# Optimization experiments

Measured on AMD Instinct MI355X. Metric: run time of the kernel, lower is better.

The kernel has to match this reference:

```python
import jax, jax.numpy as jnp
import numpy as np

N_NODES = 100000
N_EDGES = 3200000
IN_DIM = 256
OUT_DIM = 256


def setup_inputs() -> dict:
    key = jax.random.key(0)
    k1, k2, k3, k4, k5 = jax.random.split(key, 5)
    x = jax.random.normal(k1, (N_NODES, IN_DIM), dtype=jnp.float32)
    edge_src = jax.random.randint(k2, (N_EDGES,), 0, N_NODES, dtype=jnp.int32)
    edge_dst = jax.random.randint(k3, (N_EDGES,), 0, N_NODES, dtype=jnp.int32)
    # normalized adjacency values (e.g. D^-1/2 A D^-1/2 entries)
    edge_val = jax.random.uniform(k4, (N_EDGES,), dtype=jnp.float32)
    # parameters: uniform(0,1) weight, constant 0.3 bias (matches torch init)
    weight = jax.random.uniform(k5, (IN_DIM, OUT_DIM), dtype=jnp.float32)
    bias = jnp.full((OUT_DIM,), 0.3, dtype=jnp.float32)
    return {"x": x, "edge_src": edge_src, "edge_dst": edge_dst,
            "edge_val": edge_val, "weight": weight, "bias": bias}


def reference(x, edge_src, edge_dst, edge_val, weight, bias):
    # dense feature transform: [N, in] @ [in, out] -> [N, out]
    h = x @ weight
    # sparse adjacency aggregation: out[d] = sum_e val[e] * h[src[e]] for dst[e]==d
    msgs = edge_val[:, None] * h[edge_src]              # [E, out]
    agg = jax.ops.segment_sum(msgs, edge_dst, num_segments=N_NODES)
    return agg + bias
```

## Files before the change

kernel.cpp:

```cpp
#include <hip/hip_runtime.h>

#define FDIM 256
#define BSH 6
#define NBMAX 1600
#define CH 4096
#define NSLOT 7
#define CAPB 2432

typedef __attribute__((ext_vector_type(4))) float f32x4;
typedef __attribute__((ext_vector_type(8))) short bf16x8;
typedef unsigned long long u64;

static __device__ __forceinline__ unsigned short f32_to_bf16_rtn(float f) {
    unsigned u = __builtin_bit_cast(unsigned, f);
    u += 0x7FFFu + ((u >> 16) & 1u);
    return (unsigned short)(u >> 16);
}
static __device__ __forceinline__ float bf16_to_f32(unsigned short s) {
    unsigned u = ((unsigned)s) << 16;
    return __builtin_bit_cast(float, u);
}

__global__ __launch_bounds__(256) void convert_hist_kernel(
    const float* __restrict__ x, unsigned short* __restrict__ xh, long n8,
    const int* __restrict__ dst, int* __restrict__ bucket_counts, int n_edges, int nb,
    const float* __restrict__ W, unsigned short* __restrict__ wfrag) {
    __shared__ int h[NBMAX];
    for (int i = threadIdx.x; i < nb; i += 256) h[i] = 0;
    __syncthreads();

    if (blockIdx.x < 32) {
        int t = blockIdx.x * 256 + threadIdx.x;
        int lane = t & 63;
        int kt   = (t >> 6) & 7;
        int nt   = t >> 9;
        int col  = nt * 16 + (lane & 15);
        int k0   = kt * 32 + 8 * (lane >> 4);
        ushort4 o0, o1;
        o0.x = f32_to_bf16_rtn(W[(k0 + 0) * FDIM + col]);
        o0.y = f32_to_bf16_rtn(W[(k0 + 1) * FDIM + col]);
        o0.z = f32_to_bf16_rtn(W[(k0 + 2) * FDIM + col]);
        o0.w = f32_to_bf16_rtn(W[(k0 + 3) * FDIM + col]);
        o1.x = f32_to_bf16_rtn(W[(k0 + 4) * FDIM + col]);
        o1.y = f32_to_bf16_rtn(W[(k0 + 5) * FDIM + col]);
        o1.z = f32_to_bf16_rtn(W[(k0 + 6) * FDIM + col]);
        o1.w = f32_to_bf16_rtn(W[(k0 + 7) * FDIM + col]);
        ((ushort4*)(wfrag + (size_t)t * 8))[0] = o0;
        ((ushort4*)(wfrag + (size_t)t * 8))[1] = o1;
    }

    long i = (long)blockIdx.x * 256 + threadIdx.x;
    long stride = (long)gridDim.x * 256;
    for (long p = i; p < n8; p += stride) {
        const float4* q = (const float4*)(x + p * 8);
        float4 a = q[0], b = q[1];
        ushort4 o0, o1;
        o0.x = f32_to_bf16_rtn(a.x); o0.y = f32_to_bf16_rtn(a.y);
        o0.z = f32_to_bf16_rtn(a.z); o0.w = f32_to_bf16_rtn(a.w);
        o1.x = f32_to_bf16_rtn(b.x); o1.y = f32_to_bf16_rtn(b.y);
        o1.z = f32_to_bf16_rtn(b.z); o1.w = f32_to_bf16_rtn(b.w);
        ((ushort4*)(xh + p * 8))[0] = o0;
        ((ushort4*)(xh + p * 8))[1] = o1;
    }
    for (long p = i; p < n_edges; p += stride) atomicAdd(&h[dst[p] >> BSH], 1);
    __syncthreads();
    for (int b = threadIdx.x; b < nb; b += 256)
        if (h[b]) atomicAdd(&bucket_counts[b], h[b]);
}

__global__ __launch_bounds__(1024) void scan_buckets_kernel(const int* __restrict__ counts,
                                                            int* __restrict__ base,
                                                            int* __restrict__ cursor, int nb) {
    __shared__ int s[1024];
    int t = threadIdx.x;
    int i0 = 2 * t, i1 = 2 * t + 1;
    int v0 = (i0 < nb) ? counts[i0] : 0;
    int v1 = (i1 < nb) ? counts[i1] : 0;
    s[t] = v0 + v1;
    __syncthreads();
    #pragma unroll
    for (int off = 1; off < 1024; off <<= 1) {
        int u = (t >= off) ? s[t - off] : 0;
        __syncthreads();
        s[t] += u;
        __syncthreads();
    }
    int excl = s[t] - (v0 + v1);
    if (i0 < nb) { base[i0] = excl;      cursor[i0] = excl; }
    if (i1 < nb) { base[i1] = excl + v0; cursor[i1] = excl + v0; }
}

__global__ __launch_bounds__(256) void bin_kernel(
    const int* __restrict__ src, const int* __restrict__ dst, const float* __restrict__ val,
    int* __restrict__ bucket_cursor, u64* __restrict__ binned, int n_edges, int nb) {
    __shared__ int hist[NBMAX];
    __shared__ int gbase[NBMAX];
    __shared__ int sbase[NBMAX];
    __shared__ int scan_s[256];
    __shared__ u64 stage[CH];
    __shared__ unsigned short bos[CH];

    const int t = threadIdx.x;
    const int chunk0 = blockIdx.x * CH;
    const int m = min(CH, n_edges - chunk0);

    for (int b = t; b < nb; b += 256) hist[b] = 0;
    __syncthreads();
    for (int i = t; i < m; i += 256) atomicAdd(&hist[dst[chunk0 + i] >> BSH], 1);
    __syncthreads();
    for (int b = t; b < nb; b += 256) {
        int c = hist[b];
        gbase[b] = c ? atomicAdd(&bucket_cursor[b], c) : 0;
    }
    int loc[NSLOT]; int sum = 0;
    #pragma unroll
    for (int k = 0; k < NSLOT; ++k) {
        int b = t * NSLOT + k;
        int c = (b < nb) ? hist[b] : 0;
        loc[k] = sum; sum += c;
    }
    scan_s[t] = sum;
    __syncthreads();
    #pragma unroll
    for (int off = 1; off < 256; off <<= 1) {
        int u = (t >= off) ? scan_s[t - off] : 0;
        __syncthreads();
        scan_s[t] += u;
        __syncthreads();
    }
    int excl = scan_s[t] - sum;
    #pragma unroll
    for (int k = 0; k < NSLOT; ++k) {
        int b = t * NSLOT + k;
        if (b < nb) sbase[b] = excl + loc[k];
    }
    __syncthreads();
    for (int b = t; b < nb; b += 256) hist[b] = 0;
    __syncthreads();
    for (int i = t; i < m; i += 256) {
        int d = dst[chunk0 + i];
        int b = d >> BSH;
        int p = atomicAdd(&hist[b], 1);
        int slot = sbase[b] + p;
        unsigned w0 = (unsigned)src[chunk0 + i] | ((unsigned)(d & 63) << 17);
        unsigned w1 = __builtin_bit_cast(unsigned, val[chunk0 + i]);
        stage[slot] = (u64)w0 | ((u64)w1 << 32);
        bos[slot]   = (unsigned short)b;
    }
    __syncthreads();
    for (int i = t; i < m; i += 256) {
        int b = bos[i];
        binned[(size_t)gbase[b] + (i - sbase[b])] = stage[i];
    }
}

__global__ __launch_bounds__(256) void gather_kernel(
    const unsigned short* __restrict__ xh, const int* __restrict__ bucket_base,
    const int* __restrict__ bucket_counts, const u64* __restrict__ binned,
    float* __restrict__ aggf, unsigned short* __restrict__ aggb, int use_bf16, int n_nodes) {
    __shared__ u64 s2[CAPB];
    __shared__ int cnt[64], startv[64], cur[64];

    const int t = threadIdx.x, b = blockIdx.x;
    const int base = bucket_base[b];
    int m = bucket_counts[b];
    if (m > CAPB) m = CAPB;

    if (t < 64) cnt[t] = 0;
    __syncthreads();
    const unsigned* bl = (const unsigned*)(binned + base);
    for (int i = t; i < m; i += 256) atomicAdd(&cnt[(bl[2 * i] >> 17) & 63], 1);
    __syncthreads();
    if (t < 64) startv[t] = cnt[t];
    __syncthreads();
    #pragma unroll
    for (int off = 1; off < 64; off <<= 1) {
        int u = 0;
        if (t < 64 && t >= off) u = startv[t - off];
        __syncthreads();
        if (t < 64) startv[t] += u;
        __syncthreads();
    }
    if (t < 64) cur[t] = startv[t] - cnt[t];
    __syncthreads();
    for (int i = t; i < m; i += 256) {
        u64 e = binned[base + i];
        int p = atomicAdd(&cur[(int)((e >> 17) & 63)], 1);
        s2[p] = e;
    }
    __syncthreads();

    const int wv = t >> 6, lane = t & 63;
    const int half = lane >> 5, l32 = lane & 31;
    for (int q = 0; q < 16; ++q) {
        const int lo = wv * 16 + q;
        const int node = (b << BSH) + lo;
        const int beg = startv[lo] - cnt[lo];
        const int end = startv[lo];
        float acc[8] = {0.f, 0.f, 0.f, 0.f, 0.f, 0.f, 0.f, 0.f};
        int j = beg;
        for (; j + 16 <= end; j += 16) {
            #pragma unroll
            for (int k = 0; k < 8; ++k) {
                u64 e = s2[j + 2 * k + half];
                float v = __builtin_bit_cast(float, (unsigned)(e >> 32));
                bf16x8 r = *(const bf16x8*)(xh + (((size_t)((unsigned)e & 0x1FFFF)) << 8) + (l32 << 3));
                #pragma unroll
                for (int d = 0; d < 8; ++d)
                    acc[d] += v * bf16_to_f32((unsigned short)r[d]);
            }
        }
        for (; j + 8 <= end; j += 8) {
            #pragma unroll
            for (int k = 0; k < 4; ++k) {
                u64 e = s2[j + 2 * k + half];
                float v = __builtin_bit_cast(float, (unsigned)(e >> 32));
                bf16x8 r = *(const bf16x8*)(xh + (((size_t)((unsigned)e & 0x1FFFF)) << 8) + (l32 << 3));
                #pragma unroll
                for (int d = 0; d < 8; ++d)
                    acc[d] += v * bf16_to_f32((unsigned short)r[d]);
            }
        }
        for (; j < end; j += 2) {
            int idx = j + half;
            u64 e = s2[idx < end ? idx : j];
            float v = (idx < end) ? __builtin_bit_cast(float, (unsigned)(e >> 32)) : 0.f;
            bf16x8 r = *(const bf16x8*)(xh + (((size_t)((unsigned)e & 0x1FFFF)) << 8) + (l32 << 3));
            #pragma unroll
            for (int d = 0; d < 8; ++d)
                acc[d] += v * bf16_to_f32((unsigned short)r[d]);
        }
        #pragma unroll
        for (int d = 0; d < 8; ++d) acc[d] += __shfl_xor(acc[d], 32);
        if (node < n_nodes) {
            float c0 = acc[4 * half + 0], c1 = acc[4 * half + 1];
            float c2 = acc[4 * half + 2], c3 = acc[4 * half + 3];
            if (use_bf16) {
                u64 w = (u64)f32_to_bf16_rtn(c0) | ((u64)f32_to_bf16_rtn(c1) << 16)
                      | ((u64)f32_to_bf16_rtn(c2) << 32) | ((u64)f32_to_bf16_rtn(c3) << 48);
                __builtin_nontemporal_store(w,
                    (u64*)(aggb + ((size_t)node << 8) + (l32 << 3) + (half << 2)));
            } else {
                f32x4 o = {c0, c1, c2, c3};
                __builtin_nontemporal_store(o,
                    (f32x4*)(aggf + ((size_t)node << 8) + (l32 << 3) + (half << 2)));
            }
        }
    }
}

template <bool BF16A>
__global__ __launch_bounds__(256) void gemm_mfma_kernel(
    const void* __restrict__ Araw, const unsigned short* __restrict__ wfrag,
    const float* __restrict__ bias, float* __restrict__ out, int n_rows) {
    int wave = (int)((blockIdx.x * 256u + threadIdx.x) >> 6);
    int lane = threadIdx.x & 63;
    int m0 = wave * 32;
    if (m0 >= n_rows) return;

    f32x4 acc[2][16];
    #pragma unroll
    for (int s = 0; s < 2; ++s)
        #pragma unroll
        for (int i = 0; i < 16; ++i) acc[s][i] = (f32x4)(0.f);

    const int arow0 = m0 + (lane & 15);
    const int arow1 = arow0 + 16;
    const int kbase = 8 * (lane >> 4);

    #pragma unroll
    for (int kt = 0; kt < 8; ++kt) {
        bf16x8 af0, af1;
        if (BF16A) {
            const unsigned short* Ab = (const unsigned short*)Araw;
            af0 = __builtin_nontemporal_load(
                (const bf16x8*)(Ab + (size_t)arow0 * FDIM + kt * 32 + kbase));
            af1 = __builtin_nontemporal_load(
                (const bf16x8*)(Ab + (size_t)arow1 * FDIM + kt * 32 + kbase));
        } else {
            const float* A = (const float*)Araw;
            const f32x4* ap0 = (const f32x4*)(A + (size_t)arow0 * FDIM + kt * 32 + kbase);
            const f32x4* ap1 = (const f32x4*)(A + (size_t)arow1 * FDIM + kt * 32 + kbase);
            f32x4 a0 = __builtin_nontemporal_load(ap0);
            f32x4 a1 = __builtin_nontemporal_load(ap0 + 1);
            f32x4 b0 = __builtin_nontemporal_load(ap1);
            f32x4 b1 = __builtin_nontemporal_load(ap1 + 1);
            #pragma unroll
            for (int j = 0; j < 4; ++j) {
                af0[j]     = (short)f32_to_bf16_rtn(a0[j]);
                af0[j + 4] = (short)f32_to_bf16_rtn(a1[j]);
                af1[j]     = (short)f32_to_bf16_rtn(b0[j]);
                af1[j + 4] = (short)f32_to_bf16_rtn(b1[j]);
            }
        }
        #pragma unroll
        for (int nt = 0; nt < 16; ++nt) {
            bf16x8 bfr = *(const bf16x8*)(wfrag + ((size_t)(nt * 8 + kt) * 64 + lane) * 8);
            acc[0][nt] = __builtin_amdgcn_mfma_f32_16x16x32_bf16(af0, bfr, acc[0][nt], 0, 0, 0);
            acc[1][nt] = __builtin_amdgcn_mfma_f32_16x16x32_bf16(af1, bfr, acc[1][nt], 0, 0, 0);
        }
    }

    const int col = lane & 15;
    #pragma unroll
    for (int s = 0; s < 2; ++s) {
        const int rbase = m0 + s * 16 + 4 * (lane >> 4);
        #pragma unroll
        for (int nt = 0; nt < 16; ++nt) {
            float bv = bias[nt * 16 + col];
            #pragma unroll
            for (int r = 0; r < 4; ++r) {
                int row = rbase + r;
                if (row < n_rows)
                    __builtin_nontemporal_store(acc[s][nt][r] + bv,
                        &out[(size_t)row * FDIM + nt * 16 + col]);
            }
        }
    }
}

extern "C" void kernel_launch(void* const* d_in, const int* in_sizes, int n_in,
                              void* d_out, int out_size, void* d_ws, size_t ws_size,
                              hipStream_t stream) {
    const float* x    = (const float*)d_in[0];
    const int*   src  = (const int*)  d_in[1];
    const int*   dst  = (const int*)  d_in[2];
    const float* val  = (const float*)d_in[3];
    const float* W    = (const float*)d_in[4];
    const float* bias = (const float*)d_in[5];
    float* out = (float*)d_out;

    int n_nodes = in_sizes[0] / FDIM;
    int n_edges = in_sizes[1];
    int nb = (n_nodes + 63) >> BSH;

    int* bucket_counts = (int*)d_ws;
    int* bucket_base   = bucket_counts + nb;
    int* bucket_cursor = bucket_base + nb;
    size_t ioff = 3 * (size_t)nb;
    ioff = (ioff + 1) & ~(size_t)1;
    u64* binned = (u64*)((int*)d_ws + ioff);
    unsigned short* xh    = (unsigned short*)(binned + n_edges);
    unsigned short* wfrag = xh + (size_t)n_nodes * FDIM;
    unsigned short* aggb  = wfrag + 16 * 8 * 64 * 8;

    size_t need = (size_t)((char*)(aggb + (size_t)n_nodes * FDIM) - (char*)d_ws);
    int use_bf16_agg = (ws_size >= need) ? 1 : 0;

    (void)hipMemsetAsync(bucket_counts, 0, (size_t)nb * sizeof(int), stream);

    long n8 = (long)n_nodes * FDIM / 8;
    convert_hist_kernel<<<2048, 256, 0, stream>>>(x, xh, n8, dst, bucket_counts, n_edges, nb,
                                                  W, wfrag);

    scan_buckets_kernel<<<1, 1024, 0, stream>>>(bucket_counts, bucket_base, bucket_cursor, nb);

    int bin_blocks = (n_edges + CH - 1) / CH;
    bin_kernel<<<bin_blocks, 256, 0, stream>>>(src, dst, val, bucket_cursor, binned, n_edges, nb);

    gather_kernel<<<nb, 256, 0, stream>>>(xh, bucket_base, bucket_counts, binned,
                                          out, aggb, use_bf16_agg, n_nodes);

    int waves = (n_nodes + 31) / 32;
    int gemm_blocks = (waves + 3) / 4;
    if (use_bf16_agg)
        gemm_mfma_kernel<true><<<gemm_blocks, 256, 0, stream>>>((const void*)aggb, wfrag, bias, out, n_nodes);
    else
        gemm_mfma_kernel<false><<<gemm_blocks, 256, 0, stream>>>((const void*)out, wfrag, bias, out, n_nodes);
}
```

Baseline: 544.0 us.

## Fuse histogram, scan and binning into convert kernel using fixed-capacity buckets

Drops the separate global histogram and scan passes by giving each destination bucket a fixed CAPB-sized slot region, so binning can run inside the x/W bf16 conversion kernel with per-bucket atomic cursors. This removes two kernel launches and one full read of dst. The gather kernel now keeps its bucket's edges in registers (EPT per thread) instead of reading binned memory twice. The cost is a larger, sparsely filled binned buffer, and any edges beyond CAPB per bucket are silently dropped, which the old code also truncated at gather time.

Result: faster. 492.5 us (-9.5%).

```diff
diff --git a/kernel.cpp b/kernel.cpp
--- a/kernel.cpp
+++ b/kernel.cpp
@@ -6,6 +6,7 @@
 #define CH 4096
 #define NSLOT 7
 #define CAPB 2432
+#define EPT 10
 
 typedef __attribute__((ext_vector_type(4))) float f32x4;
 typedef __attribute__((ext_vector_type(8))) short bf16x8;
@@ -21,19 +22,25 @@
     return __builtin_bit_cast(float, u);
 }
 
-__global__ __launch_bounds__(256) void convert_hist_kernel(
+__global__ __launch_bounds__(256) void convert_bin_kernel(
     const float* __restrict__ x, unsigned short* __restrict__ xh, long n8,
-    const int* __restrict__ dst, int* __restrict__ bucket_counts, int n_edges, int nb,
-    const float* __restrict__ W, unsigned short* __restrict__ wfrag) {
-    __shared__ int h[NBMAX];
-    for (int i = threadIdx.x; i < nb; i += 256) h[i] = 0;
-    __syncthreads();
+    const float* __restrict__ W, unsigned short* __restrict__ wfrag,
+    const int* __restrict__ src, const int* __restrict__ dst, const float* __restrict__ val,
+    int* __restrict__ cursors, u64* __restrict__ binned, int n_edges, int nb, int bin_blocks) {
+    __shared__ int hist[NBMAX];
+    __shared__ int gbase[NBMAX];
+    __shared__ int sbase[NBMAX];
+    __shared__ int scan_s[256];
+    __shared__ u64 stage[CH];
+    __shared__ unsigned short bos[CH];
+
+    const int t = threadIdx.x;
 
     if (blockIdx.x < 32) {
-        int t = blockIdx.x * 256 + threadIdx.x;
-        int lane = t & 63;
-        int kt   = (t >> 6) & 7;
-        int nt   = t >> 9;
+        int tt = blockIdx.x * 256 + t;
+        int lane = tt & 63;
+        int kt   = (tt >> 6) & 7;
+        int nt   = tt >> 9;
         int col  = nt * 16 + (lane & 15);
         int k0   = kt * 32 + 8 * (lane >> 4);
         ushort4 o0, o1;
@@ -45,11 +52,67 @@
         o1.y = f32_to_bf16_rtn(W[(k0 + 5) * FDIM + col]);
         o1.z = f32_to_bf16_rtn(W[(k0 + 6) * FDIM + col]);
         o1.w = f32_to_bf16_rtn(W[(k0 + 7) * FDIM + col]);
-        ((ushort4*)(wfrag + (size_t)t * 8))[0] = o0;
-        ((ushort4*)(wfrag + (size_t)t * 8))[1] = o1;
-    }
-
-    long i = (long)blockIdx.x * 256 + threadIdx.x;
+        ((ushort4*)(wfrag + (size_t)tt * 8))[0] = o0;
+        ((ushort4*)(wfrag + (size_t)tt * 8))[1] = o1;
+    }
+
+    if (blockIdx.x < bin_blocks) {
+        const int chunk0 = blockIdx.x * CH;
+        const int m = min(CH, n_edges - chunk0);
+
+        for (int b = t; b < nb; b += 256) hist[b] = 0;
+        __syncthreads();
+        for (int i = t; i < m; i += 256) atomicAdd(&hist[dst[chunk0 + i] >> BSH], 1);
+        __syncthreads();
+        for (int b = t; b < nb; b += 256) {
+            int c = hist[b];
+            gbase[b] = c ? atomicAdd(&cursors[b], c) : 0;
+        }
+        int loc[NSLOT]; int sum = 0;
+        #pragma unroll
+        for (int k = 0; k < NSLOT; ++k) {
+            int b = t * NSLOT + k;
+            int c = (b < nb) ? hist[b] : 0;
+            loc[k] = sum; sum += c;
+        }
+        scan_s[t] = sum;
+        __syncthreads();
+        #pragma unroll
+        for (int off = 1; off < 256; off <<= 1) {
+            int u = (t >= off) ? scan_s[t - off] : 0;
+            __syncthreads();
+            scan_s[t] += u;
+            __syncthreads();
+        }
+        int excl = scan_s[t] - sum;
+        #pragma unroll
+        for (int k = 0; k < NSLOT; ++k) {
+            int b = t * NSLOT + k;
+            if (b < nb) sbase[b] = excl + loc[k];
+        }
+        __syncthreads();
+        for (int b = t; b < nb; b += 256) hist[b] = 0;
+        __syncthreads();
+        for (int i = t; i < m; i += 256) {
+            int d = dst[chunk0 + i];
+            int b = d >> BSH;
+            int p = atomicAdd(&hist[b], 1);
+            int slot = sbase[b] + p;
+            unsigned w0 = (unsigned)src[chunk0 + i] | ((unsigned)(d & 63) << 17);
+            unsigned w1 = __builtin_bit_cast(unsigned, val[chunk0 + i]);
+            stage[slot] = (u64)w0 | ((u64)w1 << 32);
+            bos[slot]   = (unsigned short)b;
+        }
+        __syncthreads();
+        for (int i = t; i < m; i += 256) {
+            int b = bos[i];
+            int p = gbase[b] + (i - sbase[b]);
+            if (p < CAPB)
+                binned[(size_t)b * CAPB + p] = stage[i];
+        }
+    }
+
+    long i = (long)blockIdx.x * 256 + t;
     long stride = (long)gridDim.x * 256;
     for (long p = i; p < n8; p += stride) {
         const float4* q = (const float4*)(x + p * 8);
@@ -62,114 +125,34 @@
         ((ushort4*)(xh + p * 8))[0] = o0;
         ((ushort4*)(xh + p * 8))[1] = o1;
     }
-    for (long p = i; p < n_edges; p += stride) atomicAdd(&h[dst[p] >> BSH], 1);
-    __syncthreads();
-    for (int b = threadIdx.x; b < nb; b += 256)
-        if (h[b]) atomicAdd(&bucket_counts[b], h[b]);
-}
-
-__global__ __launch_bounds__(1024) void scan_buckets_kernel(const int* __restrict__ counts,
-                                                            int* __restrict__ base,
-                                                            int* __restrict__ cursor, int nb) {
-    __shared__ int s[1024];
-    int t = threadIdx.x;
-    int i0 = 2 * t, i1 = 2 * t + 1;
-    int v0 = (i0 < nb) ? counts[i0] : 0;
-    int v1 = (i1 < nb) ? counts[i1] : 0;
-    s[t] = v0 + v1;
-    __syncthreads();
-    #pragma unroll
-    for (int off = 1; off < 1024; off <<= 1) {
-        int u = (t >= off) ? s[t - off] : 0;
-        __syncthreads();
-        s[t] += u;
-        __syncthreads();
-    }
-    int excl = s[t] - (v0 + v1);
-    if (i0 < nb) { base[i0] = excl;      cursor[i0] = excl; }
-    if (i1 < nb) { base[i1] = excl + v0; cursor[i1] = excl + v0; }
-}
-
-__global__ __launch_bounds__(256) void bin_kernel(
-    const int* __restrict__ src, const int* __restrict__ dst, const float* __restrict__ val,
-    int* __restrict__ bucket_cursor, u64* __restrict__ binned, int n_edges, int nb) {
-    __shared__ int hist[NBMAX];
-    __shared__ int gbase[NBMAX];
-    __shared__ int sbase[NBMAX];
-    __shared__ int scan_s[256];
-    __shared__ u64 stage[CH];
-    __shared__ unsigned short bos[CH];
-
-    const int t = threadIdx.x;
-    const int chunk0 = blockIdx.x * CH;
-    const int m = min(CH, n_edges - chunk0);
-
-    for (int b = t; b < nb; b += 256) hist[b] = 0;
-    __syncthreads();
-    for (int i = t; i < m; i += 256) atomicAdd(&hist[dst[chunk0 + i] >> BSH], 1);
-    __syncthreads();
-    for (int b = t; b < nb; b += 256) {
-        int c = hist[b];
-        gbase[b] = c ? atomicAdd(&bucket_cursor[b], c) : 0;
-    }
-    int loc[NSLOT]; int sum = 0;
-    #pragma unroll
-    for (int k = 0; k < NSLOT; ++k) {
-        int b = t * NSLOT + k;
-        int c = (b < nb) ? hist[b] : 0;
-        loc[k] = sum; sum += c;
-    }
-    scan_s[t] = sum;
-    __syncthreads();
-    #pragma unroll
-    for (int off = 1; off < 256; off <<= 1) {
-        int u = (t >= off) ? scan_s[t - off] : 0;
-        __syncthreads();
-        scan_s[t] += u;
-        __syncthreads();
-    }
-    int excl = scan_s[t] - sum;
-    #pragma unroll
-    for (int k = 0; k < NSLOT; ++k) {
-        int b = t * NSLOT + k;
-        if (b < nb) sbase[b] = excl + loc[k];
-    }
-    __syncthreads();
-    for (int b = t; b < nb; b += 256) hist[b] = 0;
-    __syncthreads();
-    for (int i = t; i < m; i += 256) {
-        int d = dst[chunk0 + i];
-        int b = d >> BSH;
-        int p = atomicAdd(&hist[b], 1);
-        int slot = sbase[b] + p;
-        unsigned w0 = (unsigned)src[chunk0 + i] | ((unsigned)(d & 63) << 17);
-        unsigned w1 = __builtin_bit_cast(unsigned, val[chunk0 + i]);
-        stage[slot] = (u64)w0 | ((u64)w1 << 32);
-        bos[slot]   = (unsigned short)b;
-    }
-    __syncthreads();
-    for (int i = t; i < m; i += 256) {
-        int b = bos[i];
-        binned[(size_t)gbase[b] + (i - sbase[b])] = stage[i];
-    }
 }
 
 __global__ __launch_bounds__(256) void gather_kernel(
-    const unsigned short* __restrict__ xh, const int* __restrict__ bucket_base,
-    const int* __restrict__ bucket_counts, const u64* __restrict__ binned,
+    const unsigned short* __restrict__ xh, const int* __restrict__ cursors,
+    const u64* __restrict__ binned,
     float* __restrict__ aggf, unsigned short* __restrict__ aggb, int use_bf16, int n_nodes) {
     __shared__ u64 s2[CAPB];
     __shared__ int cnt[64], startv[64], cur[64];
 
     const int t = threadIdx.x, b = blockIdx.x;
-    const int base = bucket_base[b];
-    int m = bucket_counts[b];
+    const size_t base = (size_t)b * CAPB;
+    int m = cursors[b];
     if (m > CAPB) m = CAPB;
 
     if (t < 64) cnt[t] = 0;
     __syncthreads();
-    const unsigned* bl = (const unsigned*)(binned + base);
-    for (int i = t; i < m; i += 256) atomicAdd(&cnt[(bl[2 * i] >> 17) & 63], 1);
+    u64 ereg[EPT];
+    int nmine = 0;
+    #pragma unroll
+    for (int k = 0; k < EPT; ++k) {
+        int i = t + k * 256;
+        if (i < m) {
+            u64 e = binned[base + i];
+            ereg[k] = e;
+            nmine = k + 1;
+            atomicAdd(&cnt[(int)((e >> 17) & 63)], 1);
+        }
+    }
     __syncthreads();
     if (t < 64) startv[t] = cnt[t];
     __syncthreads();
@@ -183,10 +166,13 @@
     }
     if (t < 64) cur[t] = startv[t] - cnt[t];
     __syncthreads();
-    for (int i = t; i < m; i += 256) {
-        u64 e = binned[base + i];
-        int p = atomicAdd(&cur[(int)((e >> 17) & 63)], 1);
-        s2[p] = e;
+    #pragma unroll
+    for (int k = 0; k < EPT; ++k) {
+        if (k < nmine) {
+            u64 e = ereg[k];
+            int p = atomicAdd(&cur[(int)((e >> 17) & 63)], 1);
+            s2[p] = e;
+        }
     }
     __syncthreads();
 
@@ -334,31 +320,25 @@
     int n_edges = in_sizes[1];
     int nb = (n_nodes + 63) >> BSH;
 
-    int* bucket_counts = (int*)d_ws;
-    int* bucket_base   = bucket_counts + nb;
-    int* bucket_cursor = bucket_base + nb;
-    size_t ioff = 3 * (size_t)nb;
-    ioff = (ioff + 1) & ~(size_t)1;
+    int* cursors = (int*)d_ws;
+    size_t ioff = ((size_t)nb + 1) & ~(size_t)1;
     u64* binned = (u64*)((int*)d_ws + ioff);
-    unsigned short* xh    = (unsigned short*)(binned + n_edges);
+    unsigned short* xh    = (unsigned short*)(binned + (size_t)nb * CAPB);
     unsigned short* wfrag = xh + (size_t)n_nodes * FDIM;
     unsigned short* aggb  = wfrag + 16 * 8 * 64 * 8;
 
     size_t need = (size_t)((char*)(aggb + (size_t)n_nodes * FDIM) - (char*)d_ws);
     int use_bf16_agg = (ws_size >= need) ? 1 : 0;
 
-    (void)hipMemsetAsync(bucket_counts, 0, (size_t)nb * sizeof(int), stream);
+    (void)hipMemsetAsync(cursors, 0, (size_t)nb * sizeof(int), stream);
 
     long n8 = (long)n_nodes * FDIM / 8;
-    convert_hist_kernel<<<2048, 256, 0, stream>>>(x, xh, n8, dst, bucket_counts, n_edges, nb,
-                                                  W, wfrag);
-
-    scan_buckets_kernel<<<1, 1024, 0, stream>>>(bucket_counts, bucket_base, bucket_cursor, nb);
-
     int bin_blocks = (n_edges + CH - 1) / CH;
-    bin_kernel<<<bin_blocks, 256, 0, stream>>>(src, dst, val, bucket_cursor, binned, n_edges, nb);
-
-    gather_kernel<<<nb, 256, 0, stream>>>(xh, bucket_base, bucket_counts, binned,
+    convert_bin_kernel<<<2048, 256, 0, stream>>>(x, xh, n8, W, wfrag,
+                                                 src, dst, val, cursors, binned,
+                                                 n_edges, nb, bin_blocks);
+
+    gather_kernel<<<nb, 256, 0, stream>>>(xh, cursors, binned,
                                           out, aggb, use_bf16_agg, n_nodes);
 
     int waves = (n_nodes + 31) / 32;
```
